# Kernel optimization log

Hardware: AMD Instinct MI355X
Metric: run time of the kernel (lower is better)

The kernel has to match this reference:

```python
import jax, jax.numpy as jnp
import numpy as np

N_NODES = 25000
N_EDGES = 50000
NUM_ATOMS = 26
HID = 64
EMB = 64
N_GRAPHS = 64
NUM_NN_ITER = 3


def setup_inputs() -> dict:
    key = jax.random.key(0)
    ks = jax.random.split(key, 16)

    def nrm(k, shape, s=0.1):
        return jax.random.normal(k, shape, dtype=jnp.float32) * s

    x = jax.random.uniform(ks[0], (N_NODES, NUM_ATOMS), dtype=jnp.float32)
    edge_index = jax.random.randint(ks[1], (2, N_EDGES), 0, N_NODES)
    edge_attr = jax.random.uniform(ks[2], (N_EDGES, 4), dtype=jnp.float32)
    batch = jnp.sort(jax.random.randint(ks[3], (N_NODES,), 0, N_GRAPHS))

    params = dict(
        W_in=nrm(ks[4], (NUM_ATOMS, HID)), b_in=jnp.zeros((HID,), jnp.float32),
        We1=nrm(ks[5], (4, 128)), be1=jnp.zeros((128,), jnp.float32),
        We2=nrm(ks[6], (128, HID * HID), 0.02), be2=jnp.zeros((HID * HID,), jnp.float32),
        W_root=nrm(ks[7], (HID, HID)), b_conv=jnp.zeros((HID,), jnp.float32),
        W_ih=nrm(ks[8], (3 * HID, HID)), b_ih=jnp.zeros((3 * HID,), jnp.float32),
        W_hh=nrm(ks[9], (3 * HID, HID)), b_hh=jnp.zeros((3 * HID,), jnp.float32),
        Wo1=nrm(ks[10], (HID, HID)), bo1=jnp.zeros((HID,), jnp.float32),
        Wo2=nrm(ks[11], (HID, EMB)), bo2=jnp.zeros((EMB,), jnp.float32),
        Wp=nrm(ks[12], (EMB + NUM_ATOMS, 1)), bp=jnp.zeros((1,), jnp.float32),
    )
    return {"x": x, "edge_index": edge_index, "edge_attr": edge_attr, "batch": batch, **params}


def reference(x, edge_index, edge_attr, batch,
              W_in, b_in, We1, be1, We2, be2, W_root, b_conv,
              W_ih, b_ih, W_hh, b_hh, Wo1, bo1, Wo2, bo2, Wp, bp):
    src, dst = edge_index[0], edge_index[1]
    # edge MLP -> per-edge (HID, HID) weight blocks; edge_attr is fixed so compute once
    Wedge = (jax.nn.relu(edge_attr @ We1 + be1) @ We2 + be2).reshape(-1, HID, HID)  # (E, h, h)

    out = jax.nn.relu(x @ W_in + b_in)  # (N, h)
    h = out
    for _ in range(NUM_NN_ITER):
        # NNConv (aggr='add'): root transform + gather->bmm->scatter_add
        msg = jnp.einsum('ei,eio->eo', out[src], Wedge)           # (E, h)
        agg = jax.ops.segment_sum(msg, dst, num_segments=N_NODES)  # (N, h)
        m = jax.nn.relu(out @ W_root + agg + b_conv)
        # single-step GRU cell (torch GRU equations)
        gi = m @ W_ih.T + b_ih
        gh = h @ W_hh.T + b_hh
        i_r, i_z, i_n = jnp.split(gi, 3, axis=-1)
        h_r, h_z, h_n = jnp.split(gh, 3, axis=-1)
        r = jax.nn.sigmoid(i_r + h_r)
        z = jax.nn.sigmoid(i_z + h_z)
        n = jnp.tanh(i_n + r * h_n)
        h = (1.0 - z) * n + z * h
        out = h

    o = jax.nn.relu(out @ Wo1 + bo1) @ Wo2 + bo2            # (N, EMB)
    feat = jnp.concatenate([o, x], axis=1)                  # (N, EMB + NUM_ATOMS)
    # F.normalize: row-wise L2 with eps clamp
    feat = feat / jnp.maximum(jnp.linalg.norm(feat, axis=1, keepdims=True), 1e-12)
    # scatter_mean readout over graphs
    cnt = jax.ops.segment_sum(jnp.ones((N_NODES,), jnp.float32), batch, num_segments=N_GRAPHS)
    readout = jax.ops.segment_sum(feat, batch, num_segments=N_GRAPHS) / jnp.maximum(cnt, 1.0)[:, None]
    ratio = jax.nn.sigmoid(readout @ Wp + bp)               # (G, 1)
    return feat, ratio
```

## Files before the change

kernel.cpp:

```cpp
#include <hip/hip_runtime.h>
#include <math.h>

#define NN 25000
#define NE 50000
#define NEP2 50176
#define NATOM 26
#define NUM_ITER 3
#define NCH 33
#define NPB 32
#define EB3 448
#define NWAVE 14
#define NTHR 896
#define KSP 17

typedef __attribute__((ext_vector_type(8))) short bf16x8;
typedef __attribute__((ext_vector_type(8))) unsigned short ushort8_t;
typedef __attribute__((ext_vector_type(4))) float f32x4;
union FragU { bf16x8 v; ushort4 q[2]; };

#define GLDS16(gp, lp) __builtin_amdgcn_global_load_lds( \
    (const __attribute__((address_space(1))) void*)(gp), \
    (__attribute__((address_space(3))) void*)(lp), 16, 0, 0)
#define GLDS4(gp, lp) __builtin_amdgcn_global_load_lds( \
    (const __attribute__((address_space(1))) void*)(gp), \
    (__attribute__((address_space(3))) void*)(lp), 4, 0, 0)

static __device__ __forceinline__ ushort f2bf(float f) {
  unsigned u = __float_as_uint(f);
  unsigned r = (u + 0x7FFFu + ((u >> 16) & 1u)) >> 16;
  return (ushort)r;
}
static __device__ __forceinline__ unsigned cvt_pk_bf16(float a, float b) {
  unsigned r;
  asm("v_cvt_pk_bf16_f32 %0, %1, %2" : "=v"(r) : "v"(a), "v"(b));
  return r;
}
static __device__ __forceinline__ float bflo(unsigned u) { return __uint_as_float(u << 16); }
static __device__ __forceinline__ float bfhi(unsigned u) { return __uint_as_float(u & 0xFFFF0000u); }

__global__ __launch_bounds__(256) void edge_mlp_pack_kernel(
    const float* __restrict__ ea, const float* __restrict__ We1,
    const float* __restrict__ be1, ushort* __restrict__ Upkt) {
  int t = threadIdx.x;
  int el = t & 63, seg = t >> 6;
  int e = blockIdx.x * 64 + el;
  bool valid = (e < NE);
  float a0 = 0.f, a1 = 0.f, a2 = 0.f, a3 = 0.f;
  if (valid) { a0 = ea[e * 4]; a1 = ea[e * 4 + 1]; a2 = ea[e * 4 + 2]; a3 = ea[e * 4 + 3]; }
  #pragma unroll
  for (int q = 0; q < 8; ++q) {
    int g = seg * 8 + q;
    ushort out[4];
    #pragma unroll
    for (int kk = 0; kk < 4; ++kk) {
      int k = g * 4 + kk;
      float v = be1[k];
      v = fmaf(a0, We1[k], v);
      v = fmaf(a1, We1[128 + k], v);
      v = fmaf(a2, We1[256 + k], v);
      v = fmaf(a3, We1[384 + k], v);
      out[kk] = valid ? f2bf(fmaxf(v, 0.f)) : (ushort)0;
    }
    *(ushort4*)&Upkt[((size_t)g * NEP2 + e) * 4] = *(ushort4*)out;
  }
  if (seg == 0) {
    ushort out[4] = {(ushort)(valid ? 0x3F80 : 0), 0, 0, 0};
    *(ushort4*)&Upkt[((size_t)32 * NEP2 + e) * 4] = *(ushort4*)out;
  }
}

__global__ __launch_bounds__(256) void bpk_pack_kernel(
    const float* __restrict__ We2, const float* __restrict__ be2,
    ushort* __restrict__ Bpk) {
  int idx = blockIdx.x * 256 + threadIdx.x;
  int lane = idx & 63;
  int nt = (idx >> 6) & 3;
  int ks = (idx >> 8) & 7;
  int c = idx >> 11;
  int l15 = lane & 15, lg = lane >> 4;
  int o = nt * 16 + l15;
  ushort v[8];
  #pragma unroll
  for (int j = 0; j < 8; ++j) {
    int kl = (j < 4) ? (4 * lg + j) : (12 + 4 * lg + j);
    int f = c * 256 + ks * 32 + kl;
    int k = f >> 6, i = f & 63;
    float wv = 0.f;
    if (k < 128) wv = We2[(size_t)k * 4096 + i * 64 + o];
    else if (k == 128) wv = be2[i * 64 + o];
    v[j] = f2bf(wv);
  }
  *(ushort8_t*)(Bpk + (size_t)idx * 8) = *(ushort8_t*)v;
}

__global__ __launch_bounds__(256) void nw_pack_kernel(
    const float* __restrict__ W_root, const float* __restrict__ W_ih,
    const float* __restrict__ W_hh, ushort* __restrict__ Wr_pk,
    ushort* __restrict__ Bih_pk, ushort* __restrict__ Bhh_pk) {
  int idx = blockIdx.x * 256 + threadIdx.x;
  if (idx >= 3584) return;
  int lane, nt, ks, kind;
  ushort* dstp;
  if (idx < 512)      { kind = 0; int f = idx;        lane = f & 63; nt = (f >> 6) % 4;  ks = (f >> 6) / 4;  dstp = Wr_pk  + (size_t)f * 8; }
  else if (idx < 2048){ kind = 1; int f = idx - 512;  lane = f & 63; nt = (f >> 6) % 12; ks = (f >> 6) / 12; dstp = Bih_pk + (size_t)f * 8; }
  else                { kind = 2; int f = idx - 2048; lane = f & 63; nt = (f >> 6) % 12; ks = (f >> 6) / 12; dstp = Bhh_pk + (size_t)f * 8; }
  int l15 = lane & 15, lg = lane >> 4;
  int col = nt * 16 + l15;
  ushort v[8];
  #pragma unroll
  for (int j = 0; j < 8; ++j) {
    int kl = (j < 4) ? (4 * lg + j) : (12 + 4 * lg + j);
    int i = ks * 32 + kl;
    float wv;
    if (kind == 0)      wv = W_root[i * 64 + col];
    else if (kind == 1) wv = W_ih[col * 64 + i];
    else                wv = W_hh[col * 64 + i];
    v[j] = f2bf(wv);
  }
  *(ushort8_t*)dstp = *(ushort8_t*)v;
}

__global__ __launch_bounds__(NTHR, 1) void edge_rgemm7_kernel(
    const ushort* __restrict__ Upkt, const ushort* __restrict__ Bpk,
    const float* __restrict__ hv, const int* __restrict__ src,
    const int* __restrict__ dst, float* __restrict__ agg) {
  __shared__ ushort sB[2][16384];
  __shared__ ushort sU[2][1792];
  __shared__ ushort sS[448][72];
  int tid = threadIdx.x;
  int lane = tid & 63, w = tid >> 6;
  int l15 = lane & 15, lg = lane >> 4;
  int e0 = blockIdx.x * EB3;
  int c0 = blockIdx.y * KSP;
  int c1 = (c0 + KSP < NCH) ? (c0 + KSP) : NCH;

  {
    const ushort* bs = Bpk + (size_t)c0 * 16384;
    for (int q = w; q < 32; q += NWAVE)
      GLDS16(bs + ((size_t)(q * 64) + lane) * 8, &sB[0][(size_t)(q * 64) * 8]);
    const ushort* us = Upkt + ((size_t)c0 * NEP2 + e0) * 4;
    GLDS4((const char*)us + (size_t)(w * 64 + lane) * 4, (char*)&sU[0][0] + (size_t)w * 256);
  }

  #pragma unroll
  for (int r = 0; r < 8; ++r) {
    int idx = r * NTHR + tid;
    int el = idx >> 4, part = idx & 15;
    int e = e0 + el;
    float4 v = make_float4(0.f, 0.f, 0.f, 0.f);
    if (e < NE) v = ((const float4*)hv)[(size_t)src[e] * 16 + part];
    unsigned lo = cvt_pk_bf16(v.x, v.y);
    unsigned hi = cvt_pk_bf16(v.z, v.w);
    *(uint2*)&sS[el][part * 4] = make_uint2(lo, hi);
  }
  __syncthreads();

  float4 sreg[2][2][2];
  #pragma unroll
  for (int mt = 0; mt < 2; ++mt)
    #pragma unroll
    for (int p = 0; p < 2; ++p)
      #pragma unroll
      for (int g = 0; g < 2; ++g) {
        uint2 d = *(const uint2*)&sS[w * 32 + mt * 16 + l15][p * 32 + g * 16 + 4 * lg];
        sreg[mt][p][g] = make_float4(bflo(d.x), bfhi(d.x), bflo(d.y), bfhi(d.y));
      }

  f32x4 acc[2][4];
  #pragma unroll
  for (int mt = 0; mt < 2; ++mt)
    #pragma unroll
    for (int nt = 0; nt < 4; ++nt) acc[mt][nt] = (f32x4){0.f, 0.f, 0.f, 0.f};

  for (int c = c0; c < c1; ++c) {
    int cur = (c - c0) & 1;
    bool more = (c + 1 < c1);
    if (more) {
      int nb = cur ^ 1;
      const ushort* bs = Bpk + (size_t)(c + 1) * 16384;
      for (int q = w; q < 32; q += NWAVE)
        GLDS16(bs + ((size_t)(q * 64) + lane) * 8, &sB[nb][(size_t)(q * 64) * 8]);
      const ushort* us = Upkt + ((size_t)(c + 1) * NEP2 + e0) * 4;
      GLDS4((const char*)us + (size_t)(w * 64 + lane) * 4, (char*)&sU[nb][0] + (size_t)w * 256);
    }
    float uu[2][4];
    #pragma unroll
    for (int mt = 0; mt < 2; ++mt) {
      uint2 d = *(const uint2*)&sU[cur][(w * 32 + mt * 16 + l15) * 4];
      uu[mt][0] = bflo(d.x); uu[mt][1] = bfhi(d.x);
      uu[mt][2] = bflo(d.y); uu[mt][3] = bfhi(d.y);
    }
    #pragma unroll
    for (int ks = 0; ks < 8; ++ks) {
      int p = ks & 1, ku = ks >> 1;
      bf16x8 bfr[4];
      #pragma unroll
      for (int nt = 0; nt < 4; ++nt)
        bfr[nt] = *(const bf16x8*)&sB[cur][(((size_t)ks * 4 + nt) * 64 + lane) * 8];
      #pragma unroll
      for (int mt = 0; mt < 2; ++mt) {
        float u = uu[mt][ku];
        float4 s0 = sreg[mt][p][0], s1 = sreg[mt][p][1];
        union { bf16x8 v; unsigned u32[4]; } af;
        af.u32[0] = cvt_pk_bf16(s0.x * u, s0.y * u);
        af.u32[1] = cvt_pk_bf16(s0.z * u, s0.w * u);
        af.u32[2] = cvt_pk_bf16(s1.x * u, s1.y * u);
        af.u32[3] = cvt_pk_bf16(s1.z * u, s1.w * u);
        #pragma unroll
        for (int nt = 0; nt < 4; ++nt)
          acc[mt][nt] = __builtin_amdgcn_mfma_f32_16x16x32_bf16(af.v, bfr[nt], acc[mt][nt], 0, 0, 0);
      }
    }
    __syncthreads();
  }

  #pragma unroll
  for (int mt = 0; mt < 2; ++mt) {
    #pragma unroll
    for (int rr = 0; rr < 4; ++rr) {
      int e = e0 + w * 32 + mt * 16 + lg * 4 + rr;
      if (e < NE) {
        int d = dst[e];
        #pragma unroll
        for (int nt = 0; nt < 4; ++nt)
          atomicAdd(&agg[(size_t)d * 64 + nt * 16 + l15], acc[mt][nt][rr]);
      }
    }
  }
}

__global__ __launch_bounds__(256) void node_in_kernel(
    const float* __restrict__ x, const float* __restrict__ W_in,
    const float* __restrict__ b_in, float* __restrict__ h) {
  int idx = blockIdx.x * 256 + threadIdx.x;
  if (idx >= NN * 64) return;
  int n = idx >> 6, c = idx & 63;
  float acc = b_in[c];
  #pragma unroll
  for (int j = 0; j < NATOM; ++j) acc = fmaf(x[n * NATOM + j], W_in[j * 64 + c], acc);
  h[idx] = fmaxf(acc, 0.f);
}

__global__ __launch_bounds__(256, 1) void node_update2_kernel(
    float* __restrict__ hv, const float* __restrict__ agg,
    const ushort* __restrict__ Wr_pk, const ushort* __restrict__ Bih_pk,
    const ushort* __restrict__ Bhh_pk, const float* __restrict__ b_conv,
    const float* __restrict__ b_ih, const float* __restrict__ b_hh) {
  __shared__ ushort h_lds[128][72];
  __shared__ ushort m_lds[128][72];
  int tid = threadIdx.x;
  int lane = tid & 63, w = tid >> 6;
  int l15 = lane & 15, lg = lane >> 4;
  int n0 = blockIdx.x * 128;

  #pragma unroll
  for (int r = 0; r < 8; ++r) {
    int idx = r * 256 + tid;
    int row = idx >> 4, part = idx & 15;
    int n = n0 + row;
    float4 v = make_float4(0.f, 0.f, 0.f, 0.f);
    if (n < NN) v = ((const float4*)hv)[(size_t)n * 16 + part];
    *(uint2*)&h_lds[row][part * 4] =
        make_uint2(cvt_pk_bf16(v.x, v.y), cvt_pk_bf16(v.z, v.w));
  }
  __syncthreads();

  bf16x8 ah[2][2];
  #pragma unroll
  for (int mt = 0; mt < 2; ++mt)
    #pragma unroll
    for (int ks = 0; ks < 2; ++ks) {
      int row = w * 32 + mt * 16 + l15;
      FragU f;
      f.q[0] = *(const ushort4*)&h_lds[row][ks * 32 + 4 * lg];
      f.q[1] = *(const ushort4*)&h_lds[row][ks * 32 + 16 + 4 * lg];
      ah[mt][ks] = f.v;
    }

  f32x4 accm[2][4];
  #pragma unroll
  for (int mt = 0; mt < 2; ++mt)
    #pragma unroll
    for (int nt = 0; nt < 4; ++nt) accm[mt][nt] = (f32x4){0.f, 0.f, 0.f, 0.f};
  #pragma unroll
  for (int ks = 0; ks < 2; ++ks)
    #pragma unroll
    for (int nt = 0; nt < 4; ++nt) {
      bf16x8 b = *(const bf16x8*)(Wr_pk + ((size_t)((ks * 4 + nt) * 64 + lane)) * 8);
      #pragma unroll
      for (int mt = 0; mt < 2; ++mt)
        accm[mt][nt] = __builtin_amdgcn_mfma_f32_16x16x32_bf16(ah[mt][ks], b, accm[mt][nt], 0, 0, 0);
    }
  #pragma unroll
  for (int mt = 0; mt < 2; ++mt)
    #pragma unroll
    for (int nt = 0; nt < 4; ++nt) {
      int col = nt * 16 + l15;
      float bc = b_conv[col];
      #pragma unroll
      for (int rr = 0; rr < 4; ++rr) {
        int row = w * 32 + mt * 16 + lg * 4 + rr;
        int n = n0 + row;
        float val = 0.f;
        if (n < NN) val = fmaxf(accm[mt][nt][rr] + agg[(size_t)n * 64 + col] + bc, 0.f);
        m_lds[row][col] = f2bf(val);
      }
    }
  __syncthreads();

  bf16x8 am[2][2];
  #pragma unroll
  for (int mt = 0; mt < 2; ++mt)
    #pragma unroll
    for (int ks = 0; ks < 2; ++ks) {
      int row = w * 32 + mt * 16 + l15;
      FragU f;
      f.q[0] = *(const ushort4*)&m_lds[row][ks * 32 + 4 * lg];
      f.q[1] = *(const ushort4*)&m_lds[row][ks * 32 + 16 + 4 * lg];
      am[mt][ks] = f.v;
    }

  f32x4 acc_s[2][8], acc_in[2][4], acc_hn[2][4];
  #pragma unroll
  for (int mt = 0; mt < 2; ++mt) {
    #pragma unroll
    for (int nt = 0; nt < 8; ++nt) acc_s[mt][nt] = (f32x4){0.f, 0.f, 0.f, 0.f};
    #pragma unroll
    for (int nt = 0; nt < 4; ++nt) {
      acc_in[mt][nt] = (f32x4){0.f, 0.f, 0.f, 0.f};
      acc_hn[mt][nt] = (f32x4){0.f, 0.f, 0.f, 0.f};
    }
  }
  #pragma unroll
  for (int ks = 0; ks < 2; ++ks) {
    #pragma unroll
    for (int nt = 0; nt < 8; ++nt) {
      bf16x8 bi = *(const bf16x8*)(Bih_pk + ((size_t)((ks * 12 + nt) * 64 + lane)) * 8);
      bf16x8 bh = *(const bf16x8*)(Bhh_pk + ((size_t)((ks * 12 + nt) * 64 + lane)) * 8);
      #pragma unroll
      for (int mt = 0; mt < 2; ++mt) {
        acc_s[mt][nt] = __builtin_amdgcn_mfma_f32_16x16x32_bf16(am[mt][ks], bi, acc_s[mt][nt], 0, 0, 0);
        acc_s[mt][nt] = __builtin_amdgcn_mfma_f32_16x16x32_bf16(ah[mt][ks], bh, acc_s[mt][nt], 0, 0, 0);
      }
    }
    #pragma unroll
    for (int nt = 8; nt < 12; ++nt) {
      bf16x8 bi = *(const bf16x8*)(Bih_pk + ((size_t)((ks * 12 + nt) * 64 + lane)) * 8);
      bf16x8 bh = *(const bf16x8*)(Bhh_pk + ((size_t)((ks * 12 + nt) * 64 + lane)) * 8);
      #pragma unroll
      for (int mt = 0; mt < 2; ++mt) {
        acc_in[mt][nt - 8] = __builtin_amdgcn_mfma_f32_16x16x32_bf16(am[mt][ks], bi, acc_in[mt][nt - 8], 0, 0, 0);
        acc_hn[mt][nt - 8] = __builtin_amdgcn_mfma_f32_16x16x32_bf16(ah[mt][ks], bh, acc_hn[mt][nt - 8], 0, 0, 0);
      }
    }
  }

  #pragma unroll
  for (int mt = 0; mt < 2; ++mt)
    #pragma unroll
    for (int nt = 0; nt < 4; ++nt) {
      int col = nt * 16 + l15;
      float b_sr = b_ih[col] + b_hh[col];
      float b_sz = b_ih[64 + col] + b_hh[64 + col];
      float b_in_ = b_ih[128 + col];
      float b_hn = b_hh[128 + col];
      #pragma unroll
      for (int rr = 0; rr < 4; ++rr) {
        int row = w * 32 + mt * 16 + lg * 4 + rr;
        int n = n0 + row;
        if (n >= NN) continue;
        float Sr = acc_s[mt][nt][rr] + b_sr;
        float Sz = acc_s[mt][nt + 4][rr] + b_sz;
        float vin = acc_in[mt][nt][rr] + b_in_;
        float vhn = acc_hn[mt][nt][rr] + b_hn;
        float r = 1.f / (1.f + __expf(-Sr));
        float z = 1.f / (1.f + __expf(-Sz));
        float nn = tanhf(fmaf(r, vhn, vin));
        float hp = hv[(size_t)n * 64 + col];
        hv[(size_t)n * 64 + col] = (1.f - z) * nn + z * hp;
      }
    }
}

__global__ __launch_bounds__(256) void head2_kernel(
    const float* __restrict__ hv, const float* __restrict__ x,
    const float* __restrict__ Wo1, const float* __restrict__ bo1,
    const float* __restrict__ Wo2, const float* __restrict__ bo2,
    float* __restrict__ feat) {
  __shared__ float wo1[64 * 64];
  __shared__ float wo2[64 * 64];
  __shared__ float s_row[NPB * 64];
  __shared__ float s_o1[NPB * 64];
  int tid = threadIdx.x;
  int n0 = blockIdx.x * NPB;

  for (int idx = tid; idx < 64 * 16; idx += 256) {
    ((float4*)wo1)[idx] = ((const float4*)Wo1)[idx];
    ((float4*)wo2)[idx] = ((const float4*)Wo2)[idx];
  }
  for (int idx = tid; idx < NPB * 64; idx += 256) {
    int n = n0 + (idx >> 6);
    s_row[idx] = (n < NN) ? hv[(size_t)n * 64 + (idx & 63)] : 0.f;
  }
  __syncthreads();

  int c = tid & 63, g = tid >> 6;
  #pragma unroll
  for (int q = 0; q < 8; ++q) {
    int nl = g + 4 * q;
    float a = bo1[c];
    for (int i = 0; i < 64; ++i) a = fmaf(s_row[nl * 64 + i], wo1[i * 64 + c], a);
    s_o1[nl * 64 + c] = fmaxf(a, 0.f);
  }
  __syncthreads();
  #pragma unroll
  for (int q = 0; q < 8; ++q) {
    int nl = g + 4 * q;
    int n = n0 + nl;
    float b = bo2[c];
    for (int i = 0; i < 64; ++i) b = fmaf(s_o1[nl * 64 + i], wo2[i * 64 + c], b);
    float xv = (c < NATOM && n < NN) ? x[(size_t)n * NATOM + c] : 0.f;
    float sq = b * b + xv * xv;
    #pragma unroll
    for (int off = 1; off < 64; off <<= 1) sq += __shfl_xor(sq, off);
    if (n >= NN) continue;
    float inv = 1.f / fmaxf(sqrtf(sq), 1e-12f);
    feat[(size_t)n * 90 + c] = b * inv;
    if (c < NATOM) feat[(size_t)n * 90 + 64 + c] = xv * inv;
  }
}

static __device__ __forceinline__ int lbound(const int* __restrict__ b, int v) {
  int lo = 0, hi = NN;
  while (lo < hi) { int m = (lo + hi) >> 1; if (b[m] < v) lo = m + 1; else hi = m; }
  return lo;
}

__global__ __launch_bounds__(128) void readout_kernel(
    const float* __restrict__ feat, const int* __restrict__ batch,
    float* __restrict__ readout, float* __restrict__ cnt) {
  __shared__ int bounds[2];
  int g = blockIdx.x;
  int t = threadIdx.x;
  if (t == 0) bounds[0] = lbound(batch, g);
  if (t == 1) bounds[1] = lbound(batch, g + 1);
  __syncthreads();
  int lo = bounds[0], hi = bounds[1];
  if (t < 90) {
    float a0 = 0.f, a1 = 0.f, a2 = 0.f, a3 = 0.f;
    int n = lo;
    for (; n + 3 < hi; n += 4) {
      a0 += feat[(size_t)n * 90 + t];
      a1 += feat[(size_t)(n + 1) * 90 + t];
      a2 += feat[(size_t)(n + 2) * 90 + t];
      a3 += feat[(size_t)(n + 3) * 90 + t];
    }
    for (; n < hi; ++n) a0 += feat[(size_t)n * 90 + t];
    readout[g * 90 + t] = (a0 + a1) + (a2 + a3);
  }
  if (t == 0) cnt[g] = (float)(hi - lo);
}

__global__ __launch_bounds__(64) void ratio_kernel(
    const float* __restrict__ readout, const float* __restrict__ cnt,
    const float* __restrict__ Wp, const float* __restrict__ bp,
    float* __restrict__ ratio) {
  int g = threadIdx.x;
  float c = fmaxf(cnt[g], 1.f);
  float a = bp[0];
  for (int j = 0; j < 90; ++j) a = fmaf(readout[g * 90 + j] / c, Wp[j], a);
  ratio[g] = 1.f / (1.f + __expf(-a));
}


extern "C" void kernel_launch(void* const* d_in, const int* in_sizes, int n_in,
                              void* d_out, int out_size, void* d_ws, size_t ws_size,
                              hipStream_t stream) {
  const float* x      = (const float*)d_in[0];
  const int*   ei     = (const int*)  d_in[1];
  const float* ea     = (const float*)d_in[2];
  const int*   batch  = (const int*)  d_in[3];
  const float* W_in   = (const float*)d_in[4];
  const float* b_in   = (const float*)d_in[5];
  const float* We1    = (const float*)d_in[6];
  const float* be1    = (const float*)d_in[7];
  const float* We2    = (const float*)d_in[8];
  const float* be2    = (const float*)d_in[9];
  const float* W_root = (const float*)d_in[10];
  const float* b_conv = (const float*)d_in[11];
  const float* W_ih   = (const float*)d_in[12];
  const float* b_ih   = (const float*)d_in[13];
  const float* W_hh   = (const float*)d_in[14];
  const float* b_hh   = (const float*)d_in[15];
  const float* Wo1    = (const float*)d_in[16];
  const float* bo1    = (const float*)d_in[17];
  const float* Wo2    = (const float*)d_in[18];
  const float* bo2    = (const float*)d_in[19];
  const float* Wp     = (const float*)d_in[20];
  const float* bp     = (const float*)d_in[21];

  const int* srcp = ei;
  const int* dstp = ei + NE;
  float* feat  = (float*)d_out;
  float* ratio = feat + (size_t)NN * 90;

  char* wsb = (char*)d_ws;
  ushort* Upkt   = (ushort*)(wsb + 0);
  ushort* Bpk    = (ushort*)(wsb + 13246464);
  float*  h      = (float*) (wsb + 14327808);
  float*  agg    = (float*) (wsb + 20727808);
  float*  readout= (float*) (wsb + 27127808);
  float*  cnt    = (float*) (wsb + 27150848);
  ushort* Wr_pk  = (ushort*)(wsb + 27151104);
  ushort* Bih_pk = (ushort*)(wsb + 27159296);
  ushort* Bhh_pk = (ushort*)(wsb + 27183872);

  edge_mlp_pack_kernel<<<NEP2 / 64, 256, 0, stream>>>(ea, We1, be1, Upkt);
  bpk_pack_kernel<<<(NCH * 8 * 4 * 64) / 256, 256, 0, stream>>>(We2, be2, Bpk);
  nw_pack_kernel<<<14, 256, 0, stream>>>(W_root, W_ih, W_hh, Wr_pk, Bih_pk, Bhh_pk);
  node_in_kernel<<<(NN * 64 + 255) / 256, 256, 0, stream>>>(x, W_in, b_in, h);

  for (int it = 0; it < NUM_ITER; ++it) {
    hipMemsetAsync(agg, 0, (size_t)NN * 64 * sizeof(float), stream);
    edge_rgemm7_kernel<<<dim3(NEP2 / EB3, 2), NTHR, 0, stream>>>(
        Upkt, Bpk, h, srcp, dstp, agg);
    node_update2_kernel<<<(NN + 127) / 128, 256, 0, stream>>>(
        h, agg, Wr_pk, Bih_pk, Bhh_pk, b_conv, b_ih, b_hh);
  }

  head2_kernel<<<(NN + NPB - 1) / NPB, 256, 0, stream>>>(
      h, x, Wo1, bo1, Wo2, bo2, feat);
  readout_kernel<<<64, 128, 0, stream>>>(feat, batch, readout, cnt);
  ratio_kernel<<<1, 64, 0, stream>>>(readout, cnt, Wp, bp, ratio);
}
```

Baseline: 427.1 us.

## Merge prep kernels, fold agg zeroing into node update, fuse readout and ratio

The four setup kernels (edge MLP pack, We2 pack, node weight pack, input projection) become one launch that dispatches on block index, and that launch also zeroes agg. The per-iteration memset is removed: node_update clears each agg entry right after reading it, ready for the next edge pass. Readout and ratio are merged into one kernel with a shared-memory dot-product reduction. The goal is fewer kernel launches and memset passes, at the cost of an extra store per agg element in node_update and more branching in prep.

```diff
diff --git a/kernel.cpp b/kernel.cpp
--- a/kernel.cpp
+++ b/kernel.cpp
@@ -38,86 +38,102 @@
 static __device__ __forceinline__ float bflo(unsigned u) { return __uint_as_float(u << 16); }
 static __device__ __forceinline__ float bfhi(unsigned u) { return __uint_as_float(u & 0xFFFF0000u); }
 
-__global__ __launch_bounds__(256) void edge_mlp_pack_kernel(
+#define PB_U 784
+#define PB_B (PB_U + 264)
+#define PB_NW (PB_B + 14)
+#define PB_NI (PB_NW + 6250)
+
+__global__ __launch_bounds__(256) void prep_kernel(
     const float* __restrict__ ea, const float* __restrict__ We1,
-    const float* __restrict__ be1, ushort* __restrict__ Upkt) {
-  int t = threadIdx.x;
-  int el = t & 63, seg = t >> 6;
-  int e = blockIdx.x * 64 + el;
-  bool valid = (e < NE);
-  float a0 = 0.f, a1 = 0.f, a2 = 0.f, a3 = 0.f;
-  if (valid) { a0 = ea[e * 4]; a1 = ea[e * 4 + 1]; a2 = ea[e * 4 + 2]; a3 = ea[e * 4 + 3]; }
-  #pragma unroll
-  for (int q = 0; q < 8; ++q) {
-    int g = seg * 8 + q;
-    ushort out[4];
-    #pragma unroll
-    for (int kk = 0; kk < 4; ++kk) {
-      int k = g * 4 + kk;
-      float v = be1[k];
-      v = fmaf(a0, We1[k], v);
-      v = fmaf(a1, We1[128 + k], v);
-      v = fmaf(a2, We1[256 + k], v);
-      v = fmaf(a3, We1[384 + k], v);
-      out[kk] = valid ? f2bf(fmaxf(v, 0.f)) : (ushort)0;
-    }
-    *(ushort4*)&Upkt[((size_t)g * NEP2 + e) * 4] = *(ushort4*)out;
-  }
-  if (seg == 0) {
-    ushort out[4] = {(ushort)(valid ? 0x3F80 : 0), 0, 0, 0};
-    *(ushort4*)&Upkt[((size_t)32 * NEP2 + e) * 4] = *(ushort4*)out;
-  }
-}
-
-__global__ __launch_bounds__(256) void bpk_pack_kernel(
+    const float* __restrict__ be1, ushort* __restrict__ Upkt,
     const float* __restrict__ We2, const float* __restrict__ be2,
-    ushort* __restrict__ Bpk) {
-  int idx = blockIdx.x * 256 + threadIdx.x;
-  int lane = idx & 63;
-  int nt = (idx >> 6) & 3;
-  int ks = (idx >> 8) & 7;
-  int c = idx >> 11;
-  int l15 = lane & 15, lg = lane >> 4;
-  int o = nt * 16 + l15;
-  ushort v[8];
-  #pragma unroll
-  for (int j = 0; j < 8; ++j) {
-    int kl = (j < 4) ? (4 * lg + j) : (12 + 4 * lg + j);
-    int f = c * 256 + ks * 32 + kl;
-    int k = f >> 6, i = f & 63;
-    float wv = 0.f;
-    if (k < 128) wv = We2[(size_t)k * 4096 + i * 64 + o];
-    else if (k == 128) wv = be2[i * 64 + o];
-    v[j] = f2bf(wv);
-  }
-  *(ushort8_t*)(Bpk + (size_t)idx * 8) = *(ushort8_t*)v;
-}
-
-__global__ __launch_bounds__(256) void nw_pack_kernel(
+    ushort* __restrict__ Bpk,
     const float* __restrict__ W_root, const float* __restrict__ W_ih,
     const float* __restrict__ W_hh, ushort* __restrict__ Wr_pk,
-    ushort* __restrict__ Bih_pk, ushort* __restrict__ Bhh_pk) {
-  int idx = blockIdx.x * 256 + threadIdx.x;
-  if (idx >= 3584) return;
-  int lane, nt, ks, kind;
-  ushort* dstp;
-  if (idx < 512)      { kind = 0; int f = idx;        lane = f & 63; nt = (f >> 6) % 4;  ks = (f >> 6) / 4;  dstp = Wr_pk  + (size_t)f * 8; }
-  else if (idx < 2048){ kind = 1; int f = idx - 512;  lane = f & 63; nt = (f >> 6) % 12; ks = (f >> 6) / 12; dstp = Bih_pk + (size_t)f * 8; }
-  else                { kind = 2; int f = idx - 2048; lane = f & 63; nt = (f >> 6) % 12; ks = (f >> 6) / 12; dstp = Bhh_pk + (size_t)f * 8; }
-  int l15 = lane & 15, lg = lane >> 4;
-  int col = nt * 16 + l15;
-  ushort v[8];
-  #pragma unroll
-  for (int j = 0; j < 8; ++j) {
-    int kl = (j < 4) ? (4 * lg + j) : (12 + 4 * lg + j);
-    int i = ks * 32 + kl;
-    float wv;
-    if (kind == 0)      wv = W_root[i * 64 + col];
-    else if (kind == 1) wv = W_ih[col * 64 + i];
-    else                wv = W_hh[col * 64 + i];
-    v[j] = f2bf(wv);
-  }
-  *(ushort8_t*)dstp = *(ushort8_t*)v;
+    ushort* __restrict__ Bih_pk, ushort* __restrict__ Bhh_pk,
+    const float* __restrict__ x, const float* __restrict__ W_in,
+    const float* __restrict__ b_in, float* __restrict__ h,
+    float* __restrict__ agg) {
+  int b = blockIdx.x;
+  int t = threadIdx.x;
+  if (b < PB_U) {
+    int el = t & 63, seg = t >> 6;
+    int e = b * 64 + el;
+    bool valid = (e < NE);
+    float a0 = 0.f, a1 = 0.f, a2 = 0.f, a3 = 0.f;
+    if (valid) { a0 = ea[e * 4]; a1 = ea[e * 4 + 1]; a2 = ea[e * 4 + 2]; a3 = ea[e * 4 + 3]; }
+    #pragma unroll
+    for (int q = 0; q < 8; ++q) {
+      int g = seg * 8 + q;
+      ushort out[4];
+      #pragma unroll
+      for (int kk = 0; kk < 4; ++kk) {
+        int k = g * 4 + kk;
+        float v = be1[k];
+        v = fmaf(a0, We1[k], v);
+        v = fmaf(a1, We1[128 + k], v);
+        v = fmaf(a2, We1[256 + k], v);
+        v = fmaf(a3, We1[384 + k], v);
+        out[kk] = valid ? f2bf(fmaxf(v, 0.f)) : (ushort)0;
+      }
+      *(ushort4*)&Upkt[((size_t)g * NEP2 + e) * 4] = *(ushort4*)out;
+    }
+    if (seg == 0) {
+      ushort out[4] = {(ushort)(valid ? 0x3F80 : 0), 0, 0, 0};
+      *(ushort4*)&Upkt[((size_t)32 * NEP2 + e) * 4] = *(ushort4*)out;
+    }
+  } else if (b < PB_B) {
+    int idx = (b - PB_U) * 256 + t;
+    int lane = idx & 63;
+    int nt = (idx >> 6) & 3;
+    int ks = (idx >> 8) & 7;
+    int c = idx >> 11;
+    int l15 = lane & 15, lg = lane >> 4;
+    int o = nt * 16 + l15;
+    ushort v[8];
+    #pragma unroll
+    for (int j = 0; j < 8; ++j) {
+      int kl = (j < 4) ? (4 * lg + j) : (12 + 4 * lg + j);
+      int f = c * 256 + ks * 32 + kl;
+      int k = f >> 6, i = f & 63;
+      float wv = 0.f;
+      if (k < 128) wv = We2[(size_t)k * 4096 + i * 64 + o];
+      else if (k == 128) wv = be2[i * 64 + o];
+      v[j] = f2bf(wv);
+    }
+    *(ushort8_t*)(Bpk + (size_t)idx * 8) = *(ushort8_t*)v;
+  } else if (b < PB_NW) {
+    int idx = (b - PB_B) * 256 + t;
+    if (idx >= 3584) return;
+    int lane, nt, ks, kind;
+    ushort* dstp;
+    if (idx < 512)      { kind = 0; int f = idx;        lane = f & 63; nt = (f >> 6) % 4;  ks = (f >> 6) / 4;  dstp = Wr_pk  + (size_t)f * 8; }
+    else if (idx < 2048){ kind = 1; int f = idx - 512;  lane = f & 63; nt = (f >> 6) % 12; ks = (f >> 6) / 12; dstp = Bih_pk + (size_t)f * 8; }
+    else                { kind = 2; int f = idx - 2048; lane = f & 63; nt = (f >> 6) % 12; ks = (f >> 6) / 12; dstp = Bhh_pk + (size_t)f * 8; }
+    int l15 = lane & 15, lg = lane >> 4;
+    int col = nt * 16 + l15;
+    ushort v[8];
+    #pragma unroll
+    for (int j = 0; j < 8; ++j) {
+      int kl = (j < 4) ? (4 * lg + j) : (12 + 4 * lg + j);
+      int i = ks * 32 + kl;
+      float wv;
+      if (kind == 0)      wv = W_root[i * 64 + col];
+      else if (kind == 1) wv = W_ih[col * 64 + i];
+      else                wv = W_hh[col * 64 + i];
+      v[j] = f2bf(wv);
+    }
+    *(ushort8_t*)dstp = *(ushort8_t*)v;
+  } else {
+    int idx = (b - PB_NW) * 256 + t;
+    if (idx >= NN * 64) return;
+    int n = idx >> 6, c = idx & 63;
+    float acc = b_in[c];
+    #pragma unroll
+    for (int j = 0; j < NATOM; ++j) acc = fmaf(x[n * NATOM + j], W_in[j * 64 + c], acc);
+    h[idx] = fmaxf(acc, 0.f);
+    agg[idx] = 0.f;
+  }
 }
 
 __global__ __launch_bounds__(NTHR, 1) void edge_rgemm7_kernel(
@@ -229,20 +245,8 @@
   }
 }
 
-__global__ __launch_bounds__(256) void node_in_kernel(
-    const float* __restrict__ x, const float* __restrict__ W_in,
-    const float* __restrict__ b_in, float* __restrict__ h) {
-  int idx = blockIdx.x * 256 + threadIdx.x;
-  if (idx >= NN * 64) return;
-  int n = idx >> 6, c = idx & 63;
-  float acc = b_in[c];
-  #pragma unroll
-  for (int j = 0; j < NATOM; ++j) acc = fmaf(x[n * NATOM + j], W_in[j * 64 + c], acc);
-  h[idx] = fmaxf(acc, 0.f);
-}
-
 __global__ __launch_bounds__(256, 1) void node_update2_kernel(
-    float* __restrict__ hv, const float* __restrict__ agg,
+    float* __restrict__ hv, float* __restrict__ agg,
     const ushort* __restrict__ Wr_pk, const ushort* __restrict__ Bih_pk,
     const ushort* __restrict__ Bhh_pk, const float* __restrict__ b_conv,
     const float* __restrict__ b_ih, const float* __restrict__ b_hh) {
@@ -302,7 +306,10 @@
         int row = w * 32 + mt * 16 + lg * 4 + rr;
         int n = n0 + row;
         float val = 0.f;
-        if (n < NN) val = fmaxf(accm[mt][nt][rr] + agg[(size_t)n * 64 + col] + bc, 0.f);
+        if (n < NN) {
+          val = fmaxf(accm[mt][nt][rr] + agg[(size_t)n * 64 + col] + bc, 0.f);
+          agg[(size_t)n * 64 + col] = 0.f;
+        }
         m_lds[row][col] = f2bf(val);
       }
     }
@@ -436,16 +443,19 @@
   return lo;
 }
 
-__global__ __launch_bounds__(128) void readout_kernel(
+__global__ __launch_bounds__(128) void readout_ratio_kernel(
     const float* __restrict__ feat, const int* __restrict__ batch,
-    float* __restrict__ readout, float* __restrict__ cnt) {
+    const float* __restrict__ Wp, const float* __restrict__ bp,
+    float* __restrict__ ratio) {
   __shared__ int bounds[2];
+  __shared__ float sred[128];
   int g = blockIdx.x;
   int t = threadIdx.x;
   if (t == 0) bounds[0] = lbound(batch, g);
   if (t == 1) bounds[1] = lbound(batch, g + 1);
   __syncthreads();
   int lo = bounds[0], hi = bounds[1];
+  float sum = 0.f;
   if (t < 90) {
     float a0 = 0.f, a1 = 0.f, a2 = 0.f, a3 = 0.f;
     int n = lo;
@@ -456,20 +466,20 @@
       a3 += feat[(size_t)(n + 3) * 90 + t];
     }
     for (; n < hi; ++n) a0 += feat[(size_t)n * 90 + t];
-    readout[g * 90 + t] = (a0 + a1) + (a2 + a3);
-  }
-  if (t == 0) cnt[g] = (float)(hi - lo);
-}
-
-__global__ __launch_bounds__(64) void ratio_kernel(
-    const float* __restrict__ readout, const float* __restrict__ cnt,
-    const float* __restrict__ Wp, const float* __restrict__ bp,
-    float* __restrict__ ratio) {
-  int g = threadIdx.x;
-  float c = fmaxf(cnt[g], 1.f);
-  float a = bp[0];
-  for (int j = 0; j < 90; ++j) a = fmaf(readout[g * 90 + j] / c, Wp[j], a);
-  ratio[g] = 1.f / (1.f + __expf(-a));
+    sum = (a0 + a1) + (a2 + a3);
+  }
+  sred[t] = (t < 90) ? sum * Wp[t] : 0.f;
+  __syncthreads();
+  #pragma unroll
+  for (int s = 64; s > 0; s >>= 1) {
+    if (t < s) sred[t] += sred[t + s];
+    __syncthreads();
+  }
+  if (t == 0) {
+    float c = fmaxf((float)(hi - lo), 1.f);
+    float a = sred[0] / c + bp[0];
+    ratio[g] = 1.f / (1.f + __expf(-a));
+  }
 }
 
 
@@ -509,19 +519,16 @@
   ushort* Bpk    = (ushort*)(wsb + 13246464);
   float*  h      = (float*) (wsb + 14327808);
   float*  agg    = (float*) (wsb + 20727808);
-  float*  readout= (float*) (wsb + 27127808);
-  float*  cnt    = (float*) (wsb + 27150848);
   ushort* Wr_pk  = (ushort*)(wsb + 27151104);
   ushort* Bih_pk = (ushort*)(wsb + 27159296);
   ushort* Bhh_pk = (ushort*)(wsb + 27183872);
 
-  edge_mlp_pack_kernel<<<NEP2 / 64, 256, 0, stream>>>(ea, We1, be1, Upkt);
-  bpk_pack_kernel<<<(NCH * 8 * 4 * 64) / 256, 256, 0, stream>>>(We2, be2, Bpk);
-  nw_pack_kernel<<<14, 256, 0, stream>>>(W_root, W_ih, W_hh, Wr_pk, Bih_pk, Bhh_pk);
-  node_in_kernel<<<(NN * 64 + 255) / 256, 256, 0, stream>>>(x, W_in, b_in, h);
+  prep_kernel<<<PB_NI, 256, 0, stream>>>(
+      ea, We1, be1, Upkt, We2, be2, Bpk,
+      W_root, W_ih, W_hh, Wr_pk, Bih_pk, Bhh_pk,
+      x, W_in, b_in, h, agg);
 
   for (int it = 0; it < NUM_ITER; ++it) {
-    hipMemsetAsync(agg, 0, (size_t)NN * 64 * sizeof(float), stream);
     edge_rgemm7_kernel<<<dim3(NEP2 / EB3, 2), NTHR, 0, stream>>>(
         Upkt, Bpk, h, srcp, dstp, agg);
     node_update2_kernel<<<(NN + 127) / 128, 256, 0, stream>>>(
@@ -530,6 +537,5 @@
 
   head2_kernel<<<(NN + NPB - 1) / NPB, 256, 0, stream>>>(
       h, x, Wo1, bo1, Wo2, bo2, feat);
-  readout_kernel<<<64, 128, 0, stream>>>(feat, batch, readout, cnt);
-  ratio_kernel<<<1, 64, 0, stream>>>(readout, cnt, Wp, bp, ratio);
-}
+  readout_ratio_kernel<<<64, 128, 0, stream>>>(feat, batch, Wp, bp, ratio);
+}
```

After: 400.2 us. -6.3%, faster.
